# Kernel tuning notes

Measured on AMD Instinct MI355X. Metric: run time of the kernel, lower is better.

Reference implementation:

```python
import jax, jax.numpy as jnp
import numpy as np

L = 32      # in_capsules
O = 32      # out_capsules
P = 16      # p_size
PD = 4      # p_dim = sqrt(p_size)
ETA = 1.0


def setup_inputs() -> dict:
    key = jax.random.key(0)
    k1, k2 = jax.random.split(key)
    # [B, H, W, L*16 + L]
    input_tensor = jax.random.normal(k1, (16, 14, 14, L * P + L), dtype=jnp.float32)
    # torch param: [1, K*K*L, O, 4, 4] with kernel_size=1
    weights = jax.random.normal(k2, (1, L, O, PD, PD), dtype=jnp.float32) * 0.25
    activation_bias = jnp.full((O,), 0.1, dtype=jnp.float32)
    return {"input_tensor": input_tensor, "weights": weights,
            "activation_bias": activation_bias}


def reference(input_tensor, weights, activation_bias):
    B = input_tensor.shape[0]
    # split poses / activations along channel dim
    poses_in = input_tensor[..., :-L].reshape(B, -1, PD, PD)   # [B, N, 4, 4], N = H*W*L
    acts_in = input_tensor[..., -L:].reshape(B, -1)            # [B, N]
    N = poses_in.shape[1]

    # share_transform: tile weights over spatial positions (H*W copies of the L blocks)
    w = jnp.tile(weights[0], (N // L, 1, 1, 1))                # [N, O, 4, 4]
    votes = jnp.einsum('bnij,nojk->bnoik', poses_in, w)        # [B, N, O, 4, 4]
    votes = votes.reshape(B, N, O, P)                          # [B, N, O, 16]

    # spectral routing
    votes = acts_in[:, :, None, None] * votes                  # weight by child activations
    votes = jnp.transpose(votes, (0, 2, 1, 3))                 # [B, O, N, 16]

    # top-1 right singular vector via eigendecomposition of the 16x16 gram matrix
    gram = jnp.einsum('bonp,bonq->bopq', votes, votes)         # [B, O, 16, 16]
    _, vecs = jnp.linalg.eigh(gram)                            # ascending eigenvalues
    poses = jax.lax.stop_gradient(vecs[..., -1])               # [B, O, 16] (detached, as in torch)

    yu = jnp.einsum('bonp,bop->bon', votes, poses)             # [B, O, N]
    yu_norm_sq = jnp.sum(yu * yu, axis=-1)                     # [B, O]
    y_fro_sq = jnp.sum(votes * votes, axis=(-1, -2))           # [B, O]
    activations = jax.nn.sigmoid(ETA * (yu_norm_sq / y_fro_sq - activation_bias))
    return activations, poses
```

## Files before the change

kernel.cpp:

```cpp
#include <hip/hip_runtime.h>
#include <hip/hip_bf16.h>


#define NSPAT 196

__device__ __forceinline__ float wsum64(float x) {
  x += __shfl_xor(x, 32);
  x += __shfl_xor(x, 16);
  x += __shfl_xor(x, 8);
  x += __shfl_xor(x, 4);
  x += __shfl_xor(x, 2);
  x += __shfl_xor(x, 1);
  return x;
}

__global__ __launch_bounds__(256) void moments_kernel(const float* __restrict__ in,
                                                      float* __restrict__ Mout) {
  int b = blockIdx.x >> 5;
  int l = blockIdx.x & 31;
  __shared__ float ps[NSPAT][16];
  __shared__ float as2[NSPAT];
  int t = threadIdx.x;
  for (int j = t; j < NSPAT * 16; j += 256) {
    int s = j >> 4, p = j & 15;
    ps[s][p] = in[((size_t)(b * NSPAT + s)) * 544 + l * 16 + p];
  }
  for (int s = t; s < NSPAT; s += 256) {
    float a = in[((size_t)(b * NSPAT + s)) * 544 + 512 + l];
    as2[s] = a * a;
  }
  __syncthreads();
  int p = t >> 4, q = t & 15;
  float acc = 0.f;
  for (int s = 0; s < NSPAT; ++s) {
    acc += as2[s] * (ps[s][p] * ps[s][q]);
  }
  Mout[(size_t)blockIdx.x * 256 + t] = acc;
}

__global__ __launch_bounds__(256) void gram_kernel(const float* __restrict__ Min,
                                                   const float* __restrict__ W,
                                                   float* __restrict__ Gout) {
  int b = blockIdx.x >> 5;
  int o = blockIdx.x & 31;
  int t = threadIdx.x;
  __shared__ float Ms[256];
  __shared__ float Ws[16];
  int p = t >> 4, q = t & 15;
  int i1 = p >> 2, k1 = p & 3, i2 = q >> 2, k2 = q & 3;
  float acc = 0.f;
  for (int l = 0; l < 32; ++l) {
    Ms[t] = Min[((size_t)(b * 32 + l)) * 256 + t];
    if (t < 16) Ws[t] = W[((size_t)(l * 32 + o)) * 16 + t];
    __syncthreads();
    float sub = 0.f;
    for (int j2 = 0; j2 < 4; ++j2) {
      float inner = 0.f;
      for (int j = 0; j < 4; ++j)
        inner += Ws[j * 4 + k1] * Ms[(i1 * 4 + j) * 16 + (i2 * 4 + j2)];
      sub += Ws[j2 * 4 + k2] * inner;
    }
    acc += sub;
    __syncthreads();
  }
  Gout[(size_t)blockIdx.x * 256 + t] = acc;
}

#define EPSF    5.9604645e-08f
#define EPS2F   (EPSF * EPSF)
#define SAFMINF 1.1754944e-38f

__device__ __forceinline__ float ssign(float a, float b) {
  return (b >= 0.f) ? fabsf(a) : -fabsf(a);
}

__device__ __forceinline__ float slapy2(float x, float y) {
  float xa = fabsf(x), ya = fabsf(y);
  float w = fmaxf(xa, ya), z = fminf(xa, ya);
  if (z == 0.f) return w;
  float t = z / w;
  return w * sqrtf(1.f + t * t);
}

__device__ __forceinline__ void slartg(float f, float g, float* c, float* s, float* r) {
  if (g == 0.f) {
    *c = 1.f; *s = 0.f; *r = f;
  } else if (f == 0.f) {
    *c = 0.f; *s = (g >= 0.f) ? 1.f : -1.f; *r = fabsf(g);
  } else {
    float d = sqrtf(f * f + g * g);
    *c = fabsf(f) / d;
    float rr = (f >= 0.f) ? d : -d;
    *s = g / rr;
    *r = rr;
  }
}

__device__ __forceinline__ void slaev2(float a, float b, float c,
                                       float* rt1, float* rt2, float* cs1, float* sn1) {
  float sm = a + c;
  float df = a - c;
  float adf = fabsf(df);
  float tb = b + b;
  float ab = fabsf(tb);
  float acmx, acmn;
  if (fabsf(a) > fabsf(c)) { acmx = a; acmn = c; } else { acmx = c; acmn = a; }
  float rt;
  if (adf > ab)      { float t = ab / adf; rt = adf * sqrtf(1.f + t * t); }
  else if (adf < ab) { float t = adf / ab; rt = ab * sqrtf(1.f + t * t); }
  else               { rt = ab * sqrtf(2.f); }
  int sgn1;
  if (sm < 0.f) {
    *rt1 = 0.5f * (sm - rt); sgn1 = -1;
    *rt2 = (acmx / *rt1) * acmn - (b / *rt1) * b;
  } else if (sm > 0.f) {
    *rt1 = 0.5f * (sm + rt); sgn1 = 1;
    *rt2 = (acmx / *rt1) * acmn - (b / *rt1) * b;
  } else {
    *rt1 = 0.5f * rt; *rt2 = -0.5f * rt; sgn1 = 1;
  }
  float cs; int sgn2;
  if (df >= 0.f) { cs = df + rt; sgn2 = 1; }
  else           { cs = df - rt; sgn2 = -1; }
  float acs = fabsf(cs);
  float c1, s1;
  if (acs > ab) {
    float ct = -tb / cs;
    s1 = 1.f / sqrtf(1.f + ct * ct);
    c1 = ct * s1;
  } else {
    if (ab == 0.f) { c1 = 1.f; s1 = 0.f; }
    else {
      float tn = -cs / tb;
      c1 = 1.f / sqrtf(1.f + tn * tn);
      s1 = tn * c1;
    }
  }
  if (sgn1 == sgn2) { float tn = c1; c1 = -s1; s1 = tn; }
  *cs1 = c1; *sn1 = s1;
}

__global__ __launch_bounds__(64) void eig_kernel(const float* __restrict__ G,
                                                 const float* __restrict__ bias,
                                                 float* __restrict__ out) {
  const int pid = blockIdx.x;
  const int lane = threadIdx.x;
  __shared__ float A[16][17];
  __shared__ float Zr[16][17];
  __shared__ float ddl[64][17];
  __shared__ float eel[64][17];
  __shared__ float ttl[64][17];

  for (int k = 0; k < 4; ++k) {
    int t = lane + 64 * k;
    int r = t >> 4, c = t & 15;
    int rr = r >= c ? r : c;
    int cc = r >= c ? c : r;
    A[r][c] = G[(size_t)pid * 256 + rr * 16 + cc];
    Zr[r][c] = (r == c) ? 1.f : 0.f;
  }
  float trc = (lane < 16) ? G[(size_t)pid * 256 + lane * 17] : 0.f;
  float trace = wsum64(trc);
  __syncthreads();

  for (int i = 0; i < 15; ++i) {
    float acol = (lane < 16) ? A[lane][i] : 0.f;
    float alpha = __shfl(acol, i + 1);
    float x = (lane >= i + 2 && lane < 16) ? acol : 0.f;
    float xns = wsum64(x * x);
    if (xns == 0.f) {
      eel[lane][i] = alpha;
      ttl[lane][i] = 0.f;
      continue;
    }
    float beta = (alpha >= 0.f ? -1.f : 1.f) * sqrtf(alpha * alpha + xns);
    float taui = (beta - alpha) / beta;
    float scal = 1.f / (alpha - beta);
    float vreg = 0.f;
    if (lane == i + 1) vreg = 1.f;
    else if (lane >= i + 2 && lane < 16) {
      vreg = acol * scal;
      A[lane][i] = vreg;
    }
    eel[lane][i] = beta;
    ttl[lane][i] = taui;
    float wr = 0.f;
    for (int cI = i + 1; cI < 16; ++cI) {
      float vc = __shfl(vreg, cI);
      if (lane >= i + 1 && lane < 16) wr += A[lane][cI] * vc;
    }
    wr *= taui;
    float dot = wsum64((lane >= i + 1 && lane < 16) ? wr * vreg : 0.f);
    float alpha2 = -0.5f * taui * dot;
    wr += alpha2 * vreg;
    for (int cI = i + 1; cI < 16; ++cI) {
      float wc = __shfl(wr, cI);
      float vc = __shfl(vreg, cI);
      if (lane >= i + 1 && lane < 16) A[lane][cI] -= vreg * wc + wr * vc;
    }
  }

  float di = (lane < 16) ? A[lane][lane] : 0.f;
  for (int j = 0; j < 16; ++j) ddl[lane][j] = __shfl(di, j);

  float* dd = ddl[lane];
  float* ee = eel[lane];

  int m, l, lsv, lend, lendsv;
  int jtot = 0;
  const int nmaxit = 16 * 30;
  int l1 = 0;

outer:
  if (l1 > 15) goto done;
  if (l1 > 0) ee[l1 - 1] = 0.f;
  {
    int mm;
    for (mm = l1; mm < 15; ++mm) {
      float tst = fabsf(ee[mm]);
      if (tst == 0.f) break;
      if (tst <= (sqrtf(fabsf(dd[mm])) * sqrtf(fabsf(dd[mm + 1]))) * EPSF) {
        ee[mm] = 0.f;
        break;
      }
    }
    m = mm;
  }
  l = l1; lsv = l; lend = m; lendsv = lend;
  l1 = m + 1;
  if (lend == l) goto outer;
  {
    float an = 0.f;
    for (int k2 = l; k2 <= lend; ++k2) an = fmaxf(an, fabsf(dd[k2]));
    for (int k2 = l; k2 < lend; ++k2) an = fmaxf(an, fabsf(ee[k2]));
    if (an == 0.f) goto outer;
  }
  if (fabsf(dd[lend]) < fabsf(dd[l])) { lend = lsv; l = lendsv; }

  if (lend > l) {
ql_top:
    {
      int mm;
      for (mm = l; mm < lend; ++mm) {
        float tst = ee[mm] * ee[mm];
        if (tst <= (EPS2F * fabsf(dd[mm])) * fabsf(dd[mm + 1]) + SAFMINF) break;
      }
      m = mm;
    }
    if (m < lend) ee[m] = 0.f;
    {
      float p = dd[l];
      if (m == l) {
        dd[l] = p;
        l = l + 1;
        if (l <= lend) goto ql_top;
        goto blk_done;
      }
      if (m == l + 1) {
        float rt1, rt2, c2, s2;
        slaev2(dd[l], ee[l], dd[l + 1], &rt1, &rt2, &c2, &s2);
        if (lane < 16) {
          float zj = Zr[lane][l], zj1 = Zr[lane][l + 1];
          Zr[lane][l]     = c2 * zj + s2 * zj1;
          Zr[lane][l + 1] = -s2 * zj + c2 * zj1;
        }
        dd[l] = rt1; dd[l + 1] = rt2; ee[l] = 0.f;
        l += 2;
        if (l <= lend) goto ql_top;
        goto blk_done;
      }
      if (jtot == nmaxit) goto blk_done;
      jtot++;
      float g = (dd[l + 1] - p) / (2.f * ee[l]);
      float r = slapy2(g, 1.f);
      g = dd[m] - p + ee[l] / (g + ssign(r, g));
      float s = 1.f, c = 1.f;
      p = 0.f;
      for (int i = m - 1; i >= l; --i) {
        float f = s * ee[i];
        float bb = c * ee[i];
        slartg(g, f, &c, &s, &r);
        if (i != m - 1) ee[i + 1] = r;
        g = dd[i + 1] - p;
        r = (dd[i] - g) * s + 2.f * c * bb;
        p = s * r;
        dd[i + 1] = g + p;
        g = c * r - bb;
        if (lane < 16) {
          float zj = Zr[lane][i], zj1 = Zr[lane][i + 1];
          Zr[lane][i]     = c * zj - s * zj1;
          Zr[lane][i + 1] = s * zj + c * zj1;
        }
      }
      dd[l] -= p;
      ee[l] = g;
    }
    goto ql_top;
  } else {
qr_top:
    {
      int mm;
      for (mm = l; mm > lend; --mm) {
        float tst = ee[mm - 1] * ee[mm - 1];
        if (tst <= (EPS2F * fabsf(dd[mm])) * fabsf(dd[mm - 1]) + SAFMINF) break;
      }
      m = mm;
    }
    if (m > lend) ee[m - 1] = 0.f;
    {
      float p = dd[l];
      if (m == l) {
        dd[l] = p;
        l = l - 1;
        if (l >= lend) goto qr_top;
        goto blk_done;
      }
      if (m == l - 1) {
        float rt1, rt2, c2, s2;
        slaev2(dd[l - 1], ee[l - 1], dd[l], &rt1, &rt2, &c2, &s2);
        if (lane < 16) {
          float zj = Zr[lane][l - 1], zj1 = Zr[lane][l];
          Zr[lane][l - 1] = c2 * zj + s2 * zj1;
          Zr[lane][l]     = -s2 * zj + c2 * zj1;
        }
        dd[l - 1] = rt1; dd[l] = rt2; ee[l - 1] = 0.f;
        l -= 2;
        if (l >= lend) goto qr_top;
        goto blk_done;
      }
      if (jtot == nmaxit) goto blk_done;
      jtot++;
      float g = (dd[l - 1] - p) / (2.f * ee[l - 1]);
      float r = slapy2(g, 1.f);
      g = dd[m] - p + ee[l - 1] / (g + ssign(r, g));
      float s = 1.f, c = 1.f;
      p = 0.f;
      for (int i = m; i <= l - 1; ++i) {
        float f = s * ee[i];
        float bb = c * ee[i];
        slartg(g, f, &c, &s, &r);
        if (i != m) ee[i - 1] = r;
        g = dd[i] - p;
        r = (dd[i + 1] - g) * s + 2.f * c * bb;
        p = s * r;
        dd[i] = g + p;
        g = c * r - bb;
        if (lane < 16) {
          float zj = Zr[lane][i], zj1 = Zr[lane][i + 1];
          Zr[lane][i]     = c * zj + s * zj1;
          Zr[lane][i + 1] = -s * zj + c * zj1;
        }
      }
      dd[l] -= p;
      ee[l - 1] = g;
    }
    goto qr_top;
  }
blk_done:
  goto outer;

done:;
  int kmax = 0;
  float dmax = dd[0];
  for (int j = 1; j < 16; ++j) {
    float dj = dd[j];
    if (dj > dmax) { dmax = dj; kmax = j; }
  }
  float vreg = (lane < 16) ? Zr[lane][kmax] : 0.f;
  for (int i = 14; i >= 0; --i) {
    float taui = ttl[lane][i];
    if (taui == 0.f) continue;
    float contrib;
    if (lane == i + 1) contrib = vreg;
    else if (lane >= i + 2 && lane < 16) contrib = A[lane][i] * vreg;
    else contrib = 0.f;
    float dot = wsum64(contrib);
    float td = taui * dot;
    if (lane == i + 1) vreg -= td;
    else if (lane >= i + 2 && lane < 16) vreg -= td * A[lane][i];
  }

  float act = 1.f / (1.f + expf(-(dmax / trace - bias[pid & 31])));
  if (lane == 0) out[pid] = act;
  if (lane < 16) out[512 + pid * 16 + lane] = vreg;
}

extern "C" void kernel_launch(void* const* d_in, const int* in_sizes, int n_in,
                              void* d_out, int out_size, void* d_ws, size_t ws_size,
                              hipStream_t stream) {
  const float* in   = (const float*)d_in[0];
  const float* W    = (const float*)d_in[1];
  const float* bias = (const float*)d_in[2];
  float* out = (float*)d_out;

  float* Mbuf = (float*)d_ws;
  float* Gbuf = Mbuf + 512 * 256;

  moments_kernel<<<512, 256, 0, stream>>>(in, Mbuf);
  gram_kernel<<<512, 256, 0, stream>>>(Mbuf, W, Gbuf);
  eig_kernel<<<512, 64, 0, stream>>>(Gbuf, bias, out);
}
```

Measured before the change: 269.2 us.

## Preload gram inputs to shared once; read QL scalars via readlane

The gram kernel now loads all 32 moment matrices and weight blocks into shared memory up front, which removes the 64 per-iteration barriers. The QL/QR eigen loop snapshots the diagonal and off-diagonal into registers, one element per lane, and reads them with readlane instead of per-lane LDS loads. This is meant to cut LDS latency on the serial eigen solver's critical path. It costs more shared memory per gram block (about 34KB), which may lower occupancy.

Result: faster. 259.0 us (-3.8%).

```diff
diff --git a/kernel.cpp b/kernel.cpp
--- a/kernel.cpp
+++ b/kernel.cpp
@@ -12,6 +12,10 @@
   x += __shfl_xor(x, 2);
   x += __shfl_xor(x, 1);
   return x;
+}
+
+__device__ __forceinline__ float rlanef(float x, int i) {
+  return __int_as_float(__builtin_amdgcn_readlane(__float_as_int(x), i));
 }
 
 __global__ __launch_bounds__(256) void moments_kernel(const float* __restrict__ in,
@@ -44,24 +48,25 @@
   int b = blockIdx.x >> 5;
   int o = blockIdx.x & 31;
   int t = threadIdx.x;
-  __shared__ float Ms[256];
-  __shared__ float Ws[16];
+  __shared__ float Ms[32][256];
+  __shared__ float Ws[32][16];
+  for (int l = 0; l < 32; ++l)
+    Ms[l][t] = Min[((size_t)(b * 32 + l)) * 256 + t];
+  for (int j = t; j < 32 * 16; j += 256)
+    Ws[j >> 4][j & 15] = W[((size_t)((j >> 4) * 32 + o)) * 16 + (j & 15)];
+  __syncthreads();
   int p = t >> 4, q = t & 15;
   int i1 = p >> 2, k1 = p & 3, i2 = q >> 2, k2 = q & 3;
   float acc = 0.f;
   for (int l = 0; l < 32; ++l) {
-    Ms[t] = Min[((size_t)(b * 32 + l)) * 256 + t];
-    if (t < 16) Ws[t] = W[((size_t)(l * 32 + o)) * 16 + t];
-    __syncthreads();
     float sub = 0.f;
     for (int j2 = 0; j2 < 4; ++j2) {
       float inner = 0.f;
       for (int j = 0; j < 4; ++j)
-        inner += Ws[j * 4 + k1] * Ms[(i1 * 4 + j) * 16 + (i2 * 4 + j2)];
-      sub += Ws[j2 * 4 + k2] * inner;
+        inner += Ws[l][j * 4 + k1] * Ms[l][(i1 * 4 + j) * 16 + (i2 * 4 + j2)];
+      sub += Ws[l][j2 * 4 + k2] * inner;
     }
     acc += sub;
-    __syncthreads();
   }
   Gout[(size_t)blockIdx.x * 256 + t] = acc;
 }
@@ -145,6 +150,7 @@
                                                  float* __restrict__ out) {
   const int pid = blockIdx.x;
   const int lane = threadIdx.x;
+  const int row = lane & 15;
   __shared__ float A[16][17];
   __shared__ float Zr[16][17];
   __shared__ float ddl[64][17];
@@ -205,11 +211,13 @@
 
   float* dd = ddl[lane];
   float* ee = eel[lane];
+  ee[15] = 0.f;
 
   int m, l, lsv, lend, lendsv;
   int jtot = 0;
   const int nmaxit = 16 * 30;
   int l1 = 0;
+  float dsn, esn;
 
 outer:
   if (l1 > 15) goto done;
@@ -239,11 +247,14 @@
 
   if (lend > l) {
 ql_top:
+    dsn = dd[row];
+    esn = ee[row];
     {
       int mm;
       for (mm = l; mm < lend; ++mm) {
-        float tst = ee[mm] * ee[mm];
-        if (tst <= (EPS2F * fabsf(dd[mm])) * fabsf(dd[mm + 1]) + SAFMINF) break;
+        float eI = rlanef(esn, mm);
+        float tst = eI * eI;
+        if (tst <= (EPS2F * fabsf(rlanef(dsn, mm))) * fabsf(rlanef(dsn, mm + 1)) + SAFMINF) break;
       }
       m = mm;
     }
@@ -271,18 +282,19 @@
       }
       if (jtot == nmaxit) goto blk_done;
       jtot++;
-      float g = (dd[l + 1] - p) / (2.f * ee[l]);
+      float g = (rlanef(dsn, l + 1) - p) / (2.f * rlanef(esn, l));
       float r = slapy2(g, 1.f);
-      g = dd[m] - p + ee[l] / (g + ssign(r, g));
+      g = rlanef(dsn, m) - p + rlanef(esn, l) / (g + ssign(r, g));
       float s = 1.f, c = 1.f;
       p = 0.f;
       for (int i = m - 1; i >= l; --i) {
-        float f = s * ee[i];
-        float bb = c * ee[i];
+        float eI = rlanef(esn, i);
+        float f = s * eI;
+        float bb = c * eI;
         slartg(g, f, &c, &s, &r);
         if (i != m - 1) ee[i + 1] = r;
-        g = dd[i + 1] - p;
-        r = (dd[i] - g) * s + 2.f * c * bb;
+        g = rlanef(dsn, i + 1) - p;
+        r = (rlanef(dsn, i) - g) * s + 2.f * c * bb;
         p = s * r;
         dd[i + 1] = g + p;
         g = c * r - bb;
@@ -298,11 +310,14 @@
     goto ql_top;
   } else {
 qr_top:
+    dsn = dd[row];
+    esn = ee[row];
     {
       int mm;
       for (mm = l; mm > lend; --mm) {
-        float tst = ee[mm - 1] * ee[mm - 1];
-        if (tst <= (EPS2F * fabsf(dd[mm])) * fabsf(dd[mm - 1]) + SAFMINF) break;
+        float eI = rlanef(esn, mm - 1);
+        float tst = eI * eI;
+        if (tst <= (EPS2F * fabsf(rlanef(dsn, mm))) * fabsf(rlanef(dsn, mm - 1)) + SAFMINF) break;
       }
       m = mm;
     }
@@ -330,18 +345,19 @@
       }
       if (jtot == nmaxit) goto blk_done;
       jtot++;
-      float g = (dd[l - 1] - p) / (2.f * ee[l - 1]);
+      float g = (rlanef(dsn, l - 1) - p) / (2.f * rlanef(esn, l - 1));
       float r = slapy2(g, 1.f);
-      g = dd[m] - p + ee[l - 1] / (g + ssign(r, g));
+      g = rlanef(dsn, m) - p + rlanef(esn, l - 1) / (g + ssign(r, g));
       float s = 1.f, c = 1.f;
       p = 0.f;
       for (int i = m; i <= l - 1; ++i) {
-        float f = s * ee[i];
-        float bb = c * ee[i];
+        float eI = rlanef(esn, i);
+        float f = s * eI;
+        float bb = c * eI;
         slartg(g, f, &c, &s, &r);
         if (i != m) ee[i - 1] = r;
-        g = dd[i] - p;
-        r = (dd[i + 1] - g) * s + 2.f * c * bb;
+        g = rlanef(dsn, i) - p;
+        r = (rlanef(dsn, i + 1) - g) * s + 2.f * c * bb;
         p = s * r;
         dd[i] = g + p;
         g = c * r - bb;
```
